# Optimization experiments

Measured on AMD Instinct MI355X. Metric: run time of the kernel, lower is better.

Reference implementation:

```python
import jax, jax.numpy as jnp
import numpy as np


def _proj(x_flat, w, b):
    # x_flat: (N, C, L), w: (O, C), b: (O,) -> (N, O, L)  (1x1x1 Conv3d)
    return jnp.einsum('oc,ncl->nol', w, x_flat) + b[None, :, None]


def setup_inputs() -> dict:
    key = jax.random.key(0)
    ks = jax.random.split(key, 9)
    C, Ch = 256, 128
    N, T, H, W = 2, 8, 28, 28
    s_in = 1.0 / np.sqrt(C)
    s_h = 1.0 / np.sqrt(Ch)
    return {
        'x': jax.random.normal(ks[0], (N, C, T, H, W), jnp.float32),
        'g_w': jax.random.normal(ks[1], (Ch, C), jnp.float32) * s_in,
        'g_b': jax.random.normal(ks[2], (Ch,), jnp.float32) * 0.01,
        'theta_w': jax.random.normal(ks[3], (Ch, C), jnp.float32) * s_in,
        'theta_b': jax.random.normal(ks[4], (Ch,), jnp.float32) * 0.01,
        'phi_w': jax.random.normal(ks[5], (Ch, C), jnp.float32) * s_in,
        'phi_b': jax.random.normal(ks[6], (Ch,), jnp.float32) * 0.01,
        'wz_w': jax.random.normal(ks[7], (C, Ch), jnp.float32) * s_h,
        'wz_b': jax.random.normal(ks[8], (C,), jnp.float32) * 0.01,
    }


def reference(x, g_w, g_b, theta_w, theta_b, phi_w, phi_b, wz_w, wz_b):
    N, C, T, H, W = x.shape
    L = T * H * W
    xf = x.reshape(N, C, L)                      # (N, C, L)
    g_x = _proj(xf, g_w, g_b)                    # (N, Ch, L)
    theta_x = _proj(xf, theta_w, theta_b)        # (N, Ch, L)
    phi_x = _proj(xf, phi_w, phi_b)              # (N, Ch, L)
    # f[n, i, j] = theta[n, :, i] . phi[n, :, j]
    f = jnp.einsum('nci,ncj->nij', theta_x, phi_x)  # (N, L, L)
    f = jax.nn.softmax(f, axis=-1)
    # y[n, c, i] = sum_j f[n, i, j] * g[n, c, j]
    y = jnp.einsum('nij,ncj->nci', f, g_x)          # (N, Ch, L)
    z = _proj(y, wz_w, wz_b)                        # (N, C, L)
    return z.reshape(N, C, T, H, W) + x
```

## Files before the change

### kernel.cpp

```cpp
#include <hip/hip_runtime.h>
#include <hip/hip_bf16.h>

constexpr int CIN    = 256;
constexpr int CH     = 128;
constexpr int LSEQ   = 6272;
constexpr int NBATCH = 2;
constexpr int NLCH   = NBATCH * LSEQ * CH;
constexpr int WQKV   = 384 * 256;
constexpr int WZ     = 256 * 128;
constexpr float SHIFT = 40.0f;

typedef __attribute__((ext_vector_type(8))) __bf16 bf16x8;
typedef __attribute__((ext_vector_type(4))) float  f32x4;

__device__ __forceinline__ unsigned short f2bf(float f) {
    __hip_bfloat16 h = __float2bfloat16(f);
    return *reinterpret_cast<unsigned short*>(&h);
}
__device__ __forceinline__ float us2f(unsigned short h) {
    return __uint_as_float((unsigned)h << 16);
}

union BF8 { bf16x8 v; unsigned short u[8]; };
union PU  { unsigned u[4]; bf16x8 v; };

__device__ __forceinline__ unsigned cvtpk(float a, float b) {
    unsigned r;
    asm("v_cvt_pk_bf16_f32 %0, %1, %2" : "=v"(r) : "v"(a), "v"(b));
    return r;
}
__device__ __forceinline__ void pl32swap(unsigned &a, unsigned &b) {
    asm("v_permlane32_swap_b32 %0, %1" : "+v"(a), "+v"(b));
}
__device__ __forceinline__ void pl16swap(unsigned &a, unsigned &b) {
    asm("v_permlane16_swap_b32 %0, %1" : "+v"(a), "+v"(b));
}

__device__ __forceinline__ void split8(float4 a, float4 b, bf16x8& hi, bf16x8& lo) {
    BF8 H, L;
    float f[8] = { a.x, a.y, a.z, a.w, b.x, b.y, b.z, b.w };
    #pragma unroll
    for (int p = 0; p < 8; ++p) {
        unsigned short h = f2bf(f[p]);
        H.u[p] = h;
        L.u[p] = f2bf(f[p] - us2f(h));
    }
    hi = H.v; lo = L.v;
}

#define GLDS16(g, l) __builtin_amdgcn_global_load_lds(                      \
    (const __attribute__((address_space(1))) void*)(g),                     \
    (__attribute__((address_space(3))) void*)(l), 16, 0, 0)

__global__ __launch_bounds__(256) void wprep_kernel(
    const float* __restrict__ th_w, const float* __restrict__ ph_w,
    const float* __restrict__ gw,   const float* __restrict__ wz_w,
    unsigned short* __restrict__ wsp, unsigned short* __restrict__ wzsp)
{
    const int t = threadIdx.x, b = blockIdx.x;
    if (b < 48) {
        const int e   = (b * 256 + t) * 8;
        const int gch = e >> 8, c = e & 255;
        const float* src = (gch < 128) ? th_w + ((size_t)gch << 8) + c
                         : (gch < 256) ? ph_w + ((size_t)(gch - 128) << 8) + c
                                       : gw   + ((size_t)(gch - 256) << 8) + c;
        bf16x8 hi, lo;
        split8(*(const float4*)src, *(const float4*)(src + 4), hi, lo);
        *(bf16x8*)(wsp + e)        = hi;
        *(bf16x8*)(wsp + WQKV + e) = lo;
    } else {
        const int e = ((b - 48) * 256 + t) * 8;
        bf16x8 hi, lo;
        split8(*(const float4*)(wz_w + e), *(const float4*)(wz_w + e + 4), hi, lo);
        *(bf16x8*)(wzsp + e)      = hi;
        *(bf16x8*)(wzsp + WZ + e) = lo;
    }
}

__global__ __launch_bounds__(256) void proj_kernel(
    const float* __restrict__ x, const unsigned short* __restrict__ wsp,
    const float* __restrict__ th_b, const float* __restrict__ ph_b,
    const float* __restrict__ gb,
    unsigned short* __restrict__ q, unsigned short* __restrict__ k,
    unsigned short* __restrict__ vt)
{
    constexpr int XS = 264;
    __shared__ unsigned short xhi[32][XS];
    __shared__ unsigned short xlo[32][XS];
    unsigned short (*gst)[137] = (unsigned short (*)[137])&xhi[0][0];

    const int t    = threadIdx.x;
    const int n    = blockIdx.y;
    const int l0   = blockIdx.x * 32;
    const int w    = t >> 6;
    const int lane = t & 63;
    const int lo   = lane & 15;
    const int quad = lane >> 4;

    {
        const int c = t;
        const float4* xr = (const float4*)(x + (size_t)(n * CIN + c) * LSEQ + l0);
        #pragma unroll
        for (int g4 = 0; g4 < 8; ++g4) {
            float4 v = xr[g4];
            float f[4] = { v.x, v.y, v.z, v.w };
            #pragma unroll
            for (int j = 0; j < 4; ++j) {
                unsigned short h = f2bf(f[j]);
                xhi[g4 * 4 + j][c] = h;
                xlo[g4 * 4 + j][c] = f2bf(f[j] - us2f(h));
            }
        }
    }

    const unsigned short* wrp[6]; float biasv[6];
    #pragma unroll
    for (int j = 0; j < 6; ++j) {
        int gch = 96 * w + 16 * j + lo;
        wrp[j] = wsp + (size_t)gch * CIN;
        if (gch < 128)      biasv[j] = th_b[gch];
        else if (gch < 256) biasv[j] = ph_b[gch - 128];
        else                biasv[j] = gb[gch - 256];
    }

    f32x4 acc[2][6];
    #pragma unroll
    for (int mt = 0; mt < 2; ++mt)
        #pragma unroll
        for (int j = 0; j < 6; ++j) acc[mt][j] = (f32x4){0.f, 0.f, 0.f, 0.f};

    __syncthreads();

    for (int ks = 0; ks < 8; ++ks) {
        const int k0 = ks * 32 + quad * 8;
        bf16x8 ahi[2], alo[2];
        #pragma unroll
        for (int mt = 0; mt < 2; ++mt) {
            ahi[mt] = *(const bf16x8*)&xhi[mt * 16 + lo][k0];
            alo[mt] = *(const bf16x8*)&xlo[mt * 16 + lo][k0];
        }
        #pragma unroll
        for (int j = 0; j < 6; ++j) {
            const unsigned short* p = wrp[j] + k0;
            bf16x8 bhi = *(const bf16x8*)p;
            bf16x8 blo = *(const bf16x8*)(p + WQKV);
            #pragma unroll
            for (int mt = 0; mt < 2; ++mt) {
                f32x4 a = acc[mt][j];
                a = __builtin_amdgcn_mfma_f32_16x16x32_bf16(ahi[mt], bhi, a, 0, 0, 0);
                a = __builtin_amdgcn_mfma_f32_16x16x32_bf16(alo[mt], bhi, a, 0, 0, 0);
                a = __builtin_amdgcn_mfma_f32_16x16x32_bf16(ahi[mt], blo, a, 0, 0, 0);
                acc[mt][j] = a;
            }
        }
    }

    __syncthreads();

    #pragma unroll
    for (int j = 0; j < 6; ++j) {
        const int base = 96 * w + 16 * j;
        #pragma unroll
        for (int mt = 0; mt < 2; ++mt) {
            #pragma unroll
            for (int r = 0; r < 4; ++r) {
                float val = acc[mt][j][r] + biasv[j];
                const int lrow = mt * 16 + quad * 4 + r;
                if (base < 256) {
                    unsigned short* dst = (base < 128) ? q : k;
                    const int ch = (base < 128) ? base + lo : base - 128 + lo;
                    dst[(size_t)(n * LSEQ + l0 + lrow) * CH + ch] = f2bf(val);
                } else {
                    gst[lrow][base - 256 + lo] = f2bf(val);
                }
            }
        }
    }
    __syncthreads();

    #pragma unroll
    for (int rep = 0; rep < 8; ++rep) {
        const int flat = rep * 256 + t;
        const int ch   = flat >> 4;
        const int lam  = flat & 15;
        unsigned u = (unsigned)gst[2 * lam][ch] | ((unsigned)gst[2 * lam + 1][ch] << 16);
        ((unsigned*)(vt + (size_t)(n * CH + ch) * LSEQ + l0))[lam] = u;
    }
}

__global__ __launch_bounds__(256, 2) void attn_kernel(
    const unsigned short* __restrict__ qb, const unsigned short* __restrict__ kb,
    const unsigned short* __restrict__ vtg,
    float* __restrict__ Op, float* __restrict__ lp,
    unsigned short* __restrict__ yb, int ns)
{
    constexpr int NTJ = LSEQ / 64;
    __shared__ unsigned short ks [2][64][128];
    __shared__ unsigned short vTs[2][128][64];

    const int t    = threadIdx.x;
    const int s    = blockIdx.y;
    const int n    = blockIdx.z;
    const int i0   = blockIdx.x * 128;
    const int w    = t >> 6;
    const int lane = t & 63;
    const int lo   = lane & 15;
    const int quad = lane >> 4;
    const int lom  = (lo & 7) * 4;

    const int jt0 = (s * NTJ) / ns;
    const int jt1 = ((s + 1) * NTJ) / ns;

    const unsigned short* kbase = kb  + (size_t)n * LSEQ * CH;
    const unsigned short* vbase = vtg + (size_t)n * CH * LSEQ;

    bf16x8 qfrag[2][4];
    #pragma unroll
    for (int nt = 0; nt < 2; ++nt) {
        const unsigned short* qrow =
            qb + (size_t)(n * LSEQ + i0 + 32 * w + nt * 16 + lo) * CH;
        #pragma unroll
        for (int kc = 0; kc < 4; ++kc)
            qfrag[nt][kc] = *(const bf16x8*)(qrow + kc * 32 + quad * 8);
    }

    f32x4 o_acc[2][8];
    #pragma unroll
    for (int mt = 0; mt < 2; ++mt)
        #pragma unroll
        for (int nt = 0; nt < 8; ++nt) o_acc[mt][nt] = (f32x4){0.f, 0.f, 0.f, 0.f};
    float l_r[2] = {0.f, 0.f};

    auto stage = [&](int buf, int jt) {
        const int j0 = jt * 64;
        #pragma unroll
        for (int i = 0; i < 4; ++i) {
            const int c = w * 4 + i;
            {
                const int row = c * 4 + (lane >> 4);
                const int pcol = (lane & 15) * 4;
                const int lcol = pcol ^ ((row & 7) * 4);
                const unsigned short* g = kbase + (size_t)(j0 + row) * CH + lcol * 2;
                GLDS16(g, &ks[buf][0][0] + c * 512);
            }
            {
                const int row = c * 8 + (lane >> 3);
                const int pcol = (lane & 7) * 4;
                const int lcol = pcol ^ ((row & 7) * 4);
                const unsigned short* g = vbase + (size_t)row * LSEQ + j0 + lcol * 2;
                GLDS16(g, &vTs[buf][0][0] + c * 512);
            }
        }
    };

    int buf = 0;
    stage(0, jt0);
    __syncthreads();

    for (int jt = jt0; jt < jt1; ++jt) {
        if (jt + 1 < jt1) stage(buf ^ 1, jt + 1);

        bf16x8 pfrag[2][2];
        #pragma unroll
        for (int kc2 = 0; kc2 < 2; ++kc2) {
            f32x4 sacc[2][2];
            #pragma unroll
            for (int h = 0; h < 2; ++h)
                #pragma unroll
                for (int nt = 0; nt < 2; ++nt) sacc[h][nt] = (f32x4){0.f,0.f,0.f,0.f};
            #pragma unroll
            for (int kc = 0; kc < 4; ++kc) {
                const int pcol = (kc * 16 + quad * 4) ^ lom;
                #pragma unroll
                for (int h = 0; h < 2; ++h) {
                    bf16x8 a = *(const bf16x8*)&ks[buf][(kc2 * 2 + h) * 16 + lo][pcol * 2];
                    #pragma unroll
                    for (int nt = 0; nt < 2; ++nt)
                        sacc[h][nt] = __builtin_amdgcn_mfma_f32_16x16x32_bf16(
                            a, qfrag[nt][kc], sacc[h][nt], 0, 0, 0);
                }
            }
            #pragma unroll
            for (int nt = 0; nt < 2; ++nt) {
                float e[8];
                #pragma unroll
                for (int h = 0; h < 2; ++h)
                    #pragma unroll
                    for (int r = 0; r < 4; ++r) {
                        float p = __expf(sacc[h][nt][r] - SHIFT);
                        l_r[nt] += p;
                        e[h * 4 + r] = p;
                    }
                unsigned A0 = cvtpk(e[0], e[1]);
                unsigned A1 = cvtpk(e[2], e[3]);
                unsigned B0 = cvtpk(e[4], e[5]);
                unsigned B1 = cvtpk(e[6], e[7]);
                pl32swap(A0, B0); pl16swap(A0, B0);
                pl32swap(A1, B1); pl16swap(A1, B1);
                PU pu; pu.u[0] = A0; pu.u[1] = A1; pu.u[2] = B0; pu.u[3] = B1;
                pfrag[nt][kc2] = pu.v;
            }
        }

        #pragma unroll
        for (int nt8 = 0; nt8 < 8; ++nt8) {
            #pragma unroll
            for (int kc = 0; kc < 2; ++kc) {
                const int pcol = (kc * 16 + quad * 4) ^ lom;
                bf16x8 b = *(const bf16x8*)&vTs[buf][nt8 * 16 + lo][pcol * 2];
                #pragma unroll
                for (int mt = 0; mt < 2; ++mt)
                    o_acc[mt][nt8] = __builtin_amdgcn_mfma_f32_16x16x32_bf16(
                        pfrag[mt][kc], b, o_acc[mt][nt8], 0, 0, 0);
            }
        }

        __syncthreads();
        buf ^= 1;
    }

    #pragma unroll
    for (int nt = 0; nt < 2; ++nt) {
        l_r[nt] += __shfl_xor(l_r[nt], 16);
        l_r[nt] += __shfl_xor(l_r[nt], 32);
    }

    if (Op != nullptr) {
        #pragma unroll
        for (int mt = 0; mt < 2; ++mt)
            #pragma unroll
            for (int r = 0; r < 4; ++r) {
                const int qi = i0 + 32 * w + mt * 16 + quad * 4 + r;
                const float lsum = __shfl(l_r[mt], quad * 4 + r);
                float* orow = Op + ((size_t)(n * ns + s) * LSEQ + qi) * CH;
                #pragma unroll
                for (int nt = 0; nt < 8; ++nt)
                    orow[nt * 16 + lo] = o_acc[mt][nt][r];
                if (lo == 0)
                    lp[(size_t)(n * ns + s) * LSEQ + qi] = lsum;
            }
    } else {
        #pragma unroll
        for (int mt = 0; mt < 2; ++mt)
            #pragma unroll
            for (int r = 0; r < 4; ++r) {
                const int qi = i0 + 32 * w + mt * 16 + quad * 4 + r;
                const float lsum = __shfl(l_r[mt], quad * 4 + r);
                const float inv = 1.0f / lsum;
                unsigned short* yr = yb + (size_t)(n * LSEQ + qi) * CH;
                #pragma unroll
                for (int nt = 0; nt < 8; ++nt)
                    yr[nt * 16 + lo] = f2bf(o_acc[mt][nt][r] * inv);
            }
    }
}

__global__ __launch_bounds__(256) void combine_kernel(
    const float* __restrict__ Op, const float* __restrict__ lp,
    unsigned short* __restrict__ yb, int ns)
{
    const int idx = blockIdx.x * 256 + threadIdx.x;
    const int n   = idx / (LSEQ * 32);
    const int rem = idx - n * (LSEQ * 32);
    const int l   = rem >> 5;
    const int c4  = (rem & 31) << 2;

    float4 o = make_float4(0.f, 0.f, 0.f, 0.f);
    float ls = 0.f;
    for (int s = 0; s < ns; ++s) {
        const float4 v = *(const float4*)&Op[((size_t)(n * ns + s) * LSEQ + l) * CH + c4];
        o.x += v.x; o.y += v.y; o.z += v.z; o.w += v.w;
        ls += lp[(size_t)(n * ns + s) * LSEQ + l];
    }
    const float inv = 1.0f / ls;
    unsigned r0 = (unsigned)f2bf(o.x * inv) | ((unsigned)f2bf(o.y * inv) << 16);
    unsigned r1 = (unsigned)f2bf(o.z * inv) | ((unsigned)f2bf(o.w * inv) << 16);
    uint2* dst = (uint2*)(yb + (size_t)(n * LSEQ + l) * CH + c4);
    *dst = make_uint2(r0, r1);
}

__global__ __launch_bounds__(256) void zout_kernel(
    const unsigned short* __restrict__ yb,
    const unsigned short* __restrict__ wzsp, const float* __restrict__ wz_b,
    const float* __restrict__ x, float* __restrict__ out)
{
    __shared__ unsigned short ytile[32][136];

    const int t    = threadIdx.x;
    const int n    = blockIdx.y;
    const int l0   = blockIdx.x * 32;
    const int w    = t >> 6;
    const int lane = t & 63;
    const int lo   = lane & 15;
    const int quad = lane >> 4;

    #pragma unroll
    for (int rep = 0; rep < 2; ++rep) {
        const int flat8 = rep * 256 + t;
        const int l  = flat8 >> 4;
        const int c8 = (flat8 & 15) * 8;
        uint4 v = *(const uint4*)(yb + (size_t)(n * LSEQ + l0 + l) * CH + c8);
        *(uint4*)&ytile[l][c8] = v;
    }
    __syncthreads();

    f32x4 acc[4][2];
    #pragma unroll
    for (int mt = 0; mt < 4; ++mt)
        #pragma unroll
        for (int nt = 0; nt < 2; ++nt) acc[mt][nt] = (f32x4){0.f, 0.f, 0.f, 0.f};

    #pragma unroll
    for (int ks = 0; ks < 4; ++ks) {
        const int k0 = ks * 32 + quad * 8;
        bf16x8 bfr[2];
        #pragma unroll
        for (int nt = 0; nt < 2; ++nt)
            bfr[nt] = *(const bf16x8*)&ytile[nt * 16 + lo][k0];
        #pragma unroll
        for (int mt = 0; mt < 4; ++mt) {
            const unsigned short* pa = wzsp + (size_t)(64 * w + mt * 16 + lo) * CH + k0;
            bf16x8 ahi = *(const bf16x8*)pa;
            bf16x8 alo = *(const bf16x8*)(pa + WZ);
            #pragma unroll
            for (int nt = 0; nt < 2; ++nt) {
                f32x4 a = acc[mt][nt];
                a = __builtin_amdgcn_mfma_f32_16x16x32_bf16(ahi, bfr[nt], a, 0, 0, 0);
                a = __builtin_amdgcn_mfma_f32_16x16x32_bf16(alo, bfr[nt], a, 0, 0, 0);
                acc[mt][nt] = a;
            }
        }
    }

    #pragma unroll
    for (int mt = 0; mt < 4; ++mt) {
        #pragma unroll
        for (int r = 0; r < 4; ++r) {
            const int c = 64 * w + mt * 16 + quad * 4 + r;
            const float bias = wz_b[c];
            const size_t base = (size_t)(n * CIN + c) * LSEQ + l0;
            #pragma unroll
            for (int nt = 0; nt < 2; ++nt) {
                const size_t off = base + nt * 16 + lo;
                out[off] = acc[mt][nt][r] + bias + x[off];
            }
        }
    }
}

extern "C" void kernel_launch(void* const* d_in, const int* in_sizes, int n_in,
                              void* d_out, int out_size, void* d_ws, size_t ws_size,
                              hipStream_t stream) {
    const float* x    = (const float*)d_in[0];
    const float* g_w  = (const float*)d_in[1];
    const float* g_b  = (const float*)d_in[2];
    const float* th_w = (const float*)d_in[3];
    const float* th_b = (const float*)d_in[4];
    const float* ph_w = (const float*)d_in[5];
    const float* ph_b = (const float*)d_in[6];
    const float* wz_w = (const float*)d_in[7];
    const float* wz_b = (const float*)d_in[8];
    float* out = (float*)d_out;

    unsigned short* q    = (unsigned short*)d_ws;
    unsigned short* k    = q + NLCH;
    unsigned short* vt   = k + NLCH;
    unsigned short* y    = vt + NLCH;
    unsigned short* wsp  = y + NLCH;
    unsigned short* wzsp = wsp + 2 * WQKV;

    const size_t base = ((size_t)4 * NLCH + 2 * WQKV + 2 * WZ) * 2;
    const size_t per  = (size_t)NLCH * 4 + (size_t)NBATCH * LSEQ * 4;
    int ns = 0;
    if (ws_size > base) {
        size_t cap = (ws_size - base) / per;
        ns = (cap > 4) ? 4 : (int)cap;
    }

    float* Op = (ns > 0) ? (float*)(wzsp + 2 * WZ) : nullptr;
    float* lp = (ns > 0) ? Op + (size_t)ns * NLCH : nullptr;

    wprep_kernel<<<64, 256, 0, stream>>>(th_w, ph_w, g_w, wz_w, wsp, wzsp);

    proj_kernel<<<dim3(LSEQ / 32, NBATCH), 256, 0, stream>>>(
        x, wsp, th_b, ph_b, g_b, q, k, vt);

    if (ns > 0) {
        attn_kernel<<<dim3(LSEQ / 128, ns, NBATCH), 256, 0, stream>>>(
            q, k, vt, Op, lp, y, ns);
        combine_kernel<<<(NBATCH * LSEQ * 32) / 256, 256, 0, stream>>>(Op, lp, y, ns);
    } else {
        attn_kernel<<<dim3(LSEQ / 128, 1, NBATCH), 256, 0, stream>>>(
            q, k, vt, nullptr, nullptr, y, 1);
    }

    zout_kernel<<<dim3(LSEQ / 32, NBATCH), 256, 0, stream>>>(
        y, wzsp, wz_b, x, out);
}
```

Measured before the change: 175.8 us.

## Halve attention key tile to 32 and fuse split combine into output projection

After: 186.0 us. 1.06x slower.

```diff
diff --git a/kernel.cpp b/kernel.cpp
--- a/kernel.cpp
+++ b/kernel.cpp
@@ -194,9 +194,9 @@
     float* __restrict__ Op, float* __restrict__ lp,
     unsigned short* __restrict__ yb, int ns)
 {
-    constexpr int NTJ = LSEQ / 64;
-    __shared__ unsigned short ks [2][64][128];
-    __shared__ unsigned short vTs[2][128][64];
+    constexpr int NTJ = LSEQ / 32;
+    __shared__ unsigned short ks [2][32][128];
+    __shared__ unsigned short vTs[2][128][32];
 
     const int t    = threadIdx.x;
     const int s    = blockIdx.y;
@@ -207,6 +207,7 @@
     const int lo   = lane & 15;
     const int quad = lane >> 4;
     const int lom  = (lo & 7) * 4;
+    const int lomv = ((lo >> 2) & 3) * 4;
 
     const int jt0 = (s * NTJ) / ns;
     const int jt1 = ((s + 1) * NTJ) / ns;
@@ -232,10 +233,10 @@
     float l_r[2] = {0.f, 0.f};
 
     auto stage = [&](int buf, int jt) {
-        const int j0 = jt * 64;
-        #pragma unroll
-        for (int i = 0; i < 4; ++i) {
-            const int c = w * 4 + i;
+        const int j0 = jt * 32;
+        #pragma unroll
+        for (int i = 0; i < 2; ++i) {
+            const int c = w * 2 + i;
             {
                 const int row = c * 4 + (lane >> 4);
                 const int pcol = (lane & 15) * 4;
@@ -244,9 +245,9 @@
                 GLDS16(g, &ks[buf][0][0] + c * 512);
             }
             {
-                const int row = c * 8 + (lane >> 3);
-                const int pcol = (lane & 7) * 4;
-                const int lcol = pcol ^ ((row & 7) * 4);
+                const int row = c * 16 + (lane >> 2);
+                const int pcol = (lane & 3) * 4;
+                const int lcol = pcol ^ (((row >> 2) & 3) * 4);
                 const unsigned short* g = vbase + (size_t)row * LSEQ + j0 + lcol * 2;
                 GLDS16(g, &vTs[buf][0][0] + c * 512);
             }
@@ -260,59 +261,53 @@
     for (int jt = jt0; jt < jt1; ++jt) {
         if (jt + 1 < jt1) stage(buf ^ 1, jt + 1);
 
-        bf16x8 pfrag[2][2];
-        #pragma unroll
-        for (int kc2 = 0; kc2 < 2; ++kc2) {
-            f32x4 sacc[2][2];
+        bf16x8 pfrag[2];
+        f32x4 sacc[2][2];
+        #pragma unroll
+        for (int h = 0; h < 2; ++h)
+            #pragma unroll
+            for (int nt = 0; nt < 2; ++nt) sacc[h][nt] = (f32x4){0.f,0.f,0.f,0.f};
+        #pragma unroll
+        for (int kc = 0; kc < 4; ++kc) {
+            const int pcol = (kc * 16 + quad * 4) ^ lom;
+            #pragma unroll
+            for (int h = 0; h < 2; ++h) {
+                bf16x8 a = *(const bf16x8*)&ks[buf][h * 16 + lo][pcol * 2];
+                #pragma unroll
+                for (int nt = 0; nt < 2; ++nt)
+                    sacc[h][nt] = __builtin_amdgcn_mfma_f32_16x16x32_bf16(
+                        a, qfrag[nt][kc], sacc[h][nt], 0, 0, 0);
+            }
+        }
+        #pragma unroll
+        for (int nt = 0; nt < 2; ++nt) {
+            float e[8];
             #pragma unroll
             for (int h = 0; h < 2; ++h)
                 #pragma unroll
-                for (int nt = 0; nt < 2; ++nt) sacc[h][nt] = (f32x4){0.f,0.f,0.f,0.f};
-            #pragma unroll
-            for (int kc = 0; kc < 4; ++kc) {
-                const int pcol = (kc * 16 + quad * 4) ^ lom;
-                #pragma unroll
-                for (int h = 0; h < 2; ++h) {
-                    bf16x8 a = *(const bf16x8*)&ks[buf][(kc2 * 2 + h) * 16 + lo][pcol * 2];
-                    #pragma unroll
-                    for (int nt = 0; nt < 2; ++nt)
-                        sacc[h][nt] = __builtin_amdgcn_mfma_f32_16x16x32_bf16(
-                            a, qfrag[nt][kc], sacc[h][nt], 0, 0, 0);
+                for (int r = 0; r < 4; ++r) {
+                    float p = __expf(sacc[h][nt][r] - SHIFT);
+                    l_r[nt] += p;
+                    e[h * 4 + r] = p;
                 }
-            }
-            #pragma unroll
-            for (int nt = 0; nt < 2; ++nt) {
-                float e[8];
-                #pragma unroll
-                for (int h = 0; h < 2; ++h)
-                    #pragma unroll
-                    for (int r = 0; r < 4; ++r) {
-                        float p = __expf(sacc[h][nt][r] - SHIFT);
-                        l_r[nt] += p;
-                        e[h * 4 + r] = p;
-                    }
-                unsigned A0 = cvtpk(e[0], e[1]);
-                unsigned A1 = cvtpk(e[2], e[3]);
-                unsigned B0 = cvtpk(e[4], e[5]);
-                unsigned B1 = cvtpk(e[6], e[7]);
-                pl32swap(A0, B0); pl16swap(A0, B0);
-                pl32swap(A1, B1); pl16swap(A1, B1);
-                PU pu; pu.u[0] = A0; pu.u[1] = A1; pu.u[2] = B0; pu.u[3] = B1;
-                pfrag[nt][kc2] = pu.v;
-            }
+            unsigned A0 = cvtpk(e[0], e[1]);
+            unsigned A1 = cvtpk(e[2], e[3]);
+            unsigned B0 = cvtpk(e[4], e[5]);
+            unsigned B1 = cvtpk(e[6], e[7]);
+            pl32swap(A0, B0); pl16swap(A0, B0);
+            pl32swap(A1, B1); pl16swap(A1, B1);
+            PU pu; pu.u[0] = A0; pu.u[1] = A1; pu.u[2] = B0; pu.u[3] = B1;
+            pfrag[nt] = pu.v;
         }
 
         #pragma unroll
         for (int nt8 = 0; nt8 < 8; ++nt8) {
-            #pragma unroll
-            for (int kc = 0; kc < 2; ++kc) {
-                const int pcol = (kc * 16 + quad * 4) ^ lom;
-                bf16x8 b = *(const bf16x8*)&vTs[buf][nt8 * 16 + lo][pcol * 2];
-                #pragma unroll
-                for (int mt = 0; mt < 2; ++mt)
-                    o_acc[mt][nt8] = __builtin_amdgcn_mfma_f32_16x16x32_bf16(
-                        pfrag[mt][kc], b, o_acc[mt][nt8], 0, 0, 0);
-            }
+            const int pcol = (quad * 4) ^ lomv;
+            bf16x8 b = *(const bf16x8*)&vTs[buf][nt8 * 16 + lo][pcol * 2];
+            #pragma unroll
+            for (int mt = 0; mt < 2; ++mt)
+                o_acc[mt][nt8] = __builtin_amdgcn_mfma_f32_16x16x32_bf16(
+                    pfrag[mt], b, o_acc[mt][nt8], 0, 0, 0);
         }
 
         __syncthreads();
@@ -355,36 +350,14 @@
     }
 }
 
-__global__ __launch_bounds__(256) void combine_kernel(
-    const float* __restrict__ Op, const float* __restrict__ lp,
-    unsigned short* __restrict__ yb, int ns)
-{
-    const int idx = blockIdx.x * 256 + threadIdx.x;
-    const int n   = idx / (LSEQ * 32);
-    const int rem = idx - n * (LSEQ * 32);
-    const int l   = rem >> 5;
-    const int c4  = (rem & 31) << 2;
-
-    float4 o = make_float4(0.f, 0.f, 0.f, 0.f);
-    float ls = 0.f;
-    for (int s = 0; s < ns; ++s) {
-        const float4 v = *(const float4*)&Op[((size_t)(n * ns + s) * LSEQ + l) * CH + c4];
-        o.x += v.x; o.y += v.y; o.z += v.z; o.w += v.w;
-        ls += lp[(size_t)(n * ns + s) * LSEQ + l];
-    }
-    const float inv = 1.0f / ls;
-    unsigned r0 = (unsigned)f2bf(o.x * inv) | ((unsigned)f2bf(o.y * inv) << 16);
-    unsigned r1 = (unsigned)f2bf(o.z * inv) | ((unsigned)f2bf(o.w * inv) << 16);
-    uint2* dst = (uint2*)(yb + (size_t)(n * LSEQ + l) * CH + c4);
-    *dst = make_uint2(r0, r1);
-}
-
 __global__ __launch_bounds__(256) void zout_kernel(
     const unsigned short* __restrict__ yb,
+    const float* __restrict__ Op, const float* __restrict__ lp, int ns,
     const unsigned short* __restrict__ wzsp, const float* __restrict__ wz_b,
     const float* __restrict__ x, float* __restrict__ out)
 {
     __shared__ unsigned short ytile[32][136];
+    __shared__ float linv[32];
 
     const int t    = threadIdx.x;
     const int n    = blockIdx.y;
@@ -394,13 +367,39 @@
     const int lo   = lane & 15;
     const int quad = lane >> 4;
 
-    #pragma unroll
-    for (int rep = 0; rep < 2; ++rep) {
-        const int flat8 = rep * 256 + t;
-        const int l  = flat8 >> 4;
-        const int c8 = (flat8 & 15) * 8;
-        uint4 v = *(const uint4*)(yb + (size_t)(n * LSEQ + l0 + l) * CH + c8);
-        *(uint4*)&ytile[l][c8] = v;
+    if (Op != nullptr) {
+        if (t < 32) {
+            float ls = 0.f;
+            for (int sb = 0; sb < ns; ++sb)
+                ls += lp[(size_t)(n * ns + sb) * LSEQ + l0 + t];
+            linv[t] = 1.0f / ls;
+        }
+        __syncthreads();
+        #pragma unroll
+        for (int rep = 0; rep < 4; ++rep) {
+            const int flat4 = rep * 256 + t;
+            const int l  = flat4 >> 5;
+            const int c4 = (flat4 & 31) * 4;
+            float4 o = make_float4(0.f, 0.f, 0.f, 0.f);
+            for (int sb = 0; sb < ns; ++sb) {
+                const float4 v = *(const float4*)
+                    &Op[((size_t)(n * ns + sb) * LSEQ + l0 + l) * CH + c4];
+                o.x += v.x; o.y += v.y; o.z += v.z; o.w += v.w;
+            }
+            const float iv = linv[l];
+            unsigned r0 = (unsigned)f2bf(o.x * iv) | ((unsigned)f2bf(o.y * iv) << 16);
+            unsigned r1 = (unsigned)f2bf(o.z * iv) | ((unsigned)f2bf(o.w * iv) << 16);
+            *(uint2*)&ytile[l][c4] = make_uint2(r0, r1);
+        }
+    } else {
+        #pragma unroll
+        for (int rep = 0; rep < 2; ++rep) {
+            const int flat8 = rep * 256 + t;
+            const int l  = flat8 >> 4;
+            const int c8 = (flat8 & 15) * 8;
+            uint4 v = *(const uint4*)(yb + (size_t)(n * LSEQ + l0 + l) * CH + c8);
+            *(uint4*)&ytile[l][c8] = v;
+        }
     }
     __syncthreads();
 
@@ -488,12 +487,11 @@
     if (ns > 0) {
         attn_kernel<<<dim3(LSEQ / 128, ns, NBATCH), 256, 0, stream>>>(
             q, k, vt, Op, lp, y, ns);
-        combine_kernel<<<(NBATCH * LSEQ * 32) / 256, 256, 0, stream>>>(Op, lp, y, ns);
     } else {
         attn_kernel<<<dim3(LSEQ / 128, 1, NBATCH), 256, 0, stream>>>(
             q, k, vt, nullptr, nullptr, y, 1);
     }
 
     zout_kernel<<<dim3(LSEQ / 32, NBATCH), 256, 0, stream>>>(
-        y, wzsp, wz_b, x, out);
-}
+        y, Op, lp, ns, wzsp, wz_b, x, out);
+}
```

## Store split-K attention partials in bf16 and raise split count to five

Applied to the files above, without the earlier changes.

After: 168.2 us. 1.05x faster.

```diff
diff --git a/kernel.cpp b/kernel.cpp
--- a/kernel.cpp
+++ b/kernel.cpp
@@ -191,7 +191,7 @@
 __global__ __launch_bounds__(256, 2) void attn_kernel(
     const unsigned short* __restrict__ qb, const unsigned short* __restrict__ kb,
     const unsigned short* __restrict__ vtg,
-    float* __restrict__ Op, float* __restrict__ lp,
+    unsigned short* __restrict__ Op, float* __restrict__ lp,
     unsigned short* __restrict__ yb, int ns)
 {
     constexpr int NTJ = LSEQ / 64;
@@ -332,10 +332,10 @@
             for (int r = 0; r < 4; ++r) {
                 const int qi = i0 + 32 * w + mt * 16 + quad * 4 + r;
                 const float lsum = __shfl(l_r[mt], quad * 4 + r);
-                float* orow = Op + ((size_t)(n * ns + s) * LSEQ + qi) * CH;
+                unsigned short* orow = Op + ((size_t)(n * ns + s) * LSEQ + qi) * CH;
                 #pragma unroll
                 for (int nt = 0; nt < 8; ++nt)
-                    orow[nt * 16 + lo] = o_acc[mt][nt][r];
+                    orow[nt * 16 + lo] = f2bf(o_acc[mt][nt][r]);
                 if (lo == 0)
                     lp[(size_t)(n * ns + s) * LSEQ + qi] = lsum;
             }
@@ -356,27 +356,34 @@
 }
 
 __global__ __launch_bounds__(256) void combine_kernel(
-    const float* __restrict__ Op, const float* __restrict__ lp,
+    const unsigned short* __restrict__ Op, const float* __restrict__ lp,
     unsigned short* __restrict__ yb, int ns)
 {
     const int idx = blockIdx.x * 256 + threadIdx.x;
-    const int n   = idx / (LSEQ * 32);
-    const int rem = idx - n * (LSEQ * 32);
-    const int l   = rem >> 5;
-    const int c4  = (rem & 31) << 2;
-
-    float4 o = make_float4(0.f, 0.f, 0.f, 0.f);
+    const int n   = idx / (LSEQ * 16);
+    const int rem = idx - n * (LSEQ * 16);
+    const int l   = rem >> 4;
+    const int c8  = (rem & 15) << 3;
+
+    float o[8] = {0.f,0.f,0.f,0.f,0.f,0.f,0.f,0.f};
     float ls = 0.f;
     for (int s = 0; s < ns; ++s) {
-        const float4 v = *(const float4*)&Op[((size_t)(n * ns + s) * LSEQ + l) * CH + c4];
-        o.x += v.x; o.y += v.y; o.z += v.z; o.w += v.w;
+        const uint4 v = *(const uint4*)
+            &Op[((size_t)(n * ns + s) * LSEQ + l) * CH + c8];
+        const unsigned u[4] = { v.x, v.y, v.z, v.w };
+        #pragma unroll
+        for (int p = 0; p < 4; ++p) {
+            o[2 * p]     += __uint_as_float(u[p] << 16);
+            o[2 * p + 1] += __uint_as_float(u[p] & 0xffff0000u);
+        }
         ls += lp[(size_t)(n * ns + s) * LSEQ + l];
     }
     const float inv = 1.0f / ls;
-    unsigned r0 = (unsigned)f2bf(o.x * inv) | ((unsigned)f2bf(o.y * inv) << 16);
-    unsigned r1 = (unsigned)f2bf(o.z * inv) | ((unsigned)f2bf(o.w * inv) << 16);
-    uint2* dst = (uint2*)(yb + (size_t)(n * LSEQ + l) * CH + c4);
-    *dst = make_uint2(r0, r1);
+    unsigned r[4];
+    #pragma unroll
+    for (int p = 0; p < 4; ++p)
+        r[p] = (unsigned)f2bf(o[2 * p] * inv) | ((unsigned)f2bf(o[2 * p + 1] * inv) << 16);
+    *(uint4*)(yb + (size_t)(n * LSEQ + l) * CH + c8) = make_uint4(r[0], r[1], r[2], r[3]);
 }
 
 __global__ __launch_bounds__(256) void zout_kernel(
@@ -470,15 +477,15 @@
     unsigned short* wzsp = wsp + 2 * WQKV;
 
     const size_t base = ((size_t)4 * NLCH + 2 * WQKV + 2 * WZ) * 2;
-    const size_t per  = (size_t)NLCH * 4 + (size_t)NBATCH * LSEQ * 4;
+    const size_t per  = (size_t)NLCH * 2 + (size_t)NBATCH * LSEQ * 4;
     int ns = 0;
     if (ws_size > base) {
         size_t cap = (ws_size - base) / per;
-        ns = (cap > 4) ? 4 : (int)cap;
-    }
-
-    float* Op = (ns > 0) ? (float*)(wzsp + 2 * WZ) : nullptr;
-    float* lp = (ns > 0) ? Op + (size_t)ns * NLCH : nullptr;
+        ns = (cap > 5) ? 5 : (int)cap;
+    }
+
+    unsigned short* Op = (ns > 0) ? (wzsp + 2 * WZ) : nullptr;
+    float* lp = (ns > 0) ? (float*)(Op + (size_t)ns * NLCH) : nullptr;
 
     wprep_kernel<<<64, 256, 0, stream>>>(th_w, ph_w, g_w, wz_w, wsp, wzsp);
 
@@ -488,7 +495,7 @@
     if (ns > 0) {
         attn_kernel<<<dim3(LSEQ / 128, ns, NBATCH), 256, 0, stream>>>(
             q, k, vt, Op, lp, y, ns);
-        combine_kernel<<<(NBATCH * LSEQ * 32) / 256, 256, 0, stream>>>(Op, lp, y, ns);
+        combine_kernel<<<(NBATCH * LSEQ * 16) / 256, 256, 0, stream>>>(Op, lp, y, ns);
     } else {
         attn_kernel<<<dim3(LSEQ / 128, 1, NBATCH), 256, 0, stream>>>(
             q, k, vt, nullptr, nullptr, y, 1);
```
